# Kernel optimization log

Hardware: AMD Instinct MI355X
Metric: run time of the kernel (lower is better)

The kernel has to match this reference:

```python
import jax, jax.numpy as jnp
import numpy as np

N_NODES = 100000


def _sage_conv(x, src, dst, W_l, W_r, b):
    # mean aggregation of neighbor features over incoming edges (src -> dst)
    msgs = x[src]                                            # [E, d] gather
    agg = jax.ops.segment_sum(msgs, dst, num_segments=N_NODES)
    deg = jax.ops.segment_sum(jnp.ones_like(dst, dtype=x.dtype), dst,
                              num_segments=N_NODES)
    mean = agg / jnp.maximum(deg, 1.0)[:, None]              # [N, d]
    # PyG SAGEConv: lin_l(aggr) + lin_r(x); bias lives in lin_l
    return mean @ W_l + x @ W_r + b


def setup_inputs() -> dict:
    key = jax.random.key(0)
    k = jax.random.split(key, 8)
    d_in, d_h, E = 128, 128, 1600000
    scale_in = 1.0 / np.sqrt(d_in)
    scale_h = 1.0 / np.sqrt(d_h)
    return {
        "x": jax.random.normal(k[0], (N_NODES, d_in), dtype=jnp.float32),
        "edge_index": jax.random.randint(k[1], (2, E), 0, N_NODES, dtype=jnp.int64),
        "W_l0": jax.random.uniform(k[2], (d_in, d_h), jnp.float32, -scale_in, scale_in),
        "W_r0": jax.random.uniform(k[3], (d_in, d_h), jnp.float32, -scale_in, scale_in),
        "b0": jnp.zeros((d_h,), jnp.float32),
        "W_l1": jax.random.uniform(k[4], (d_h, d_h), jnp.float32, -scale_h, scale_h),
        "W_r1": jax.random.uniform(k[5], (d_h, d_h), jnp.float32, -scale_h, scale_h),
        "b1": jnp.zeros((d_h,), jnp.float32),
    }


def reference(x, edge_index, W_l0, W_r0, b0, W_l1, W_r1, b1):
    src, dst = edge_index[0], edge_index[1]
    h = _sage_conv(x, src, dst, W_l0, W_r0, b0)
    h = jax.nn.relu(h)  # dropout p=0.0 / eval mode -> identity
    h = _sage_conv(h, src, dst, W_l1, W_r1, b1)
    return h
```

## Files before the change

### kernel.cpp

```cpp
#include <hip/hip_runtime.h>


using bf16x8 = __attribute__((ext_vector_type(8))) __bf16;
using f32x4  = __attribute__((ext_vector_type(4))) float;

__device__ __forceinline__ unsigned short f2bf(float f) {
    __bf16 b = (__bf16)f;
    return __builtin_bit_cast(unsigned short, b);
}
__device__ __forceinline__ unsigned pk2(float a, float b) {
    return (unsigned)f2bf(a) | ((unsigned)f2bf(b) << 16);
}
__device__ __forceinline__ float bf2f(unsigned u16) {
    unsigned v = u16 << 16;
    return __builtin_bit_cast(float, v);
}

__device__ __forceinline__ int exscan1024(int v, int* wsum, int t) {
    int lane = t & 63, w = t >> 6;
    int x = v;
#pragma unroll
    for (int s = 1; s < 64; s <<= 1) {
        int y = __shfl_up(x, s);
        if (lane >= s) x += y;
    }
    if (lane == 63) wsum[w] = x;
    __syncthreads();
    if (w == 0) {
        int ws = (lane < 16) ? wsum[lane] : 0;
#pragma unroll
        for (int s = 1; s < 16; s <<= 1) {
            int y = __shfl_up(ws, s);
            if (lane >= s) ws += y;
        }
        if (lane < 16) wsum[lane] = ws;
    }
    __syncthreads();
    int base = (w > 0) ? wsum[w - 1] : 0;
    return base + x - v;
}


__global__ __launch_bounds__(256) void k_cvt(const float4* __restrict__ x,
                                             uint4* __restrict__ xb8,
                                             int nvec, int* __restrict__ ghist, int nb)
{
    int i = blockIdx.x * 256 + threadIdx.x;
    if (i < nb) ghist[i] = 0;
    if (i >= nvec) return;
    float4 a = x[2 * i], b = x[2 * i + 1];
    uint4 o;
    o.x = pk2(a.x, a.y);
    o.y = pk2(a.z, a.w);
    o.z = pk2(b.x, b.y);
    o.w = pk2(b.z, b.w);
    xb8[i] = o;
}


__global__ __launch_bounds__(256) void k_cvtw(const float* __restrict__ W0,
                                              const float* __restrict__ W1,
                                              const float* __restrict__ W2,
                                              const float* __restrict__ W3,
                                              unsigned short* __restrict__ wsw)
{
    int id = blockIdx.x * 256 + threadIdx.x;
    int m = id >> 14, r = id & 16383;
    int c = r >> 7, k = r & 127;
    const float* W = (m == 0) ? W0 : (m == 1) ? W1 : (m == 2) ? W2 : W3;
    wsw[m * 16384 + c * 128 + (k ^ ((c & 7) << 3))] = f2bf(W[k * 128 + c]);
}


__global__ __launch_bounds__(256) void k_binhist(const int* __restrict__ dst, int E,
                                                 int* __restrict__ ghist, int nb)
{
    __shared__ int lh[800];
    for (int i = threadIdx.x; i < nb; i += 256) lh[i] = 0;
    __syncthreads();
    for (int e = blockIdx.x * 256 + threadIdx.x; e < E; e += gridDim.x * 256)
        atomicAdd(&lh[dst[e] >> 7], 1);
    __syncthreads();
    for (int i = threadIdx.x; i < nb; i += 256)
        if (lh[i]) atomicAdd(&ghist[i], lh[i]);
}


__global__ __launch_bounds__(1024) void k_binscan(const int* __restrict__ ghist,
                                                  int* __restrict__ gbase,
                                                  int* __restrict__ gcur,
                                                  int* __restrict__ row_start,
                                                  int nb, int n, int E)
{
    __shared__ int wsum[16];
    int t = threadIdx.x;
    int v = (t < nb) ? ghist[t] : 0;
    int excl = exscan1024(v, wsum, t);
    if (t < nb) { gbase[t] = excl; gcur[t] = excl; }
    if (t == 0) { gbase[nb] = E; row_start[n] = E; }
}


#define SC_CHUNK 8192

__global__ __launch_bounds__(1024) void k_binscatter(const int* __restrict__ src,
                                                     const int* __restrict__ dst, int E,
                                                     int* __restrict__ gcur,
                                                     unsigned* __restrict__ binned, int nb)
{
    __shared__ int lh[800];
    __shared__ int lbase[800];
    __shared__ int gb[800];
    __shared__ int wsum[16];
    __shared__ unsigned long long staged[SC_CHUNK];
    int t = threadIdx.x;
    int e0 = blockIdx.x * SC_CHUNK;
    if (e0 >= E) return;
    int ecnt = E - e0; if (ecnt > SC_CHUNK) ecnt = SC_CHUNK;

    for (int i = t; i < nb; i += 1024) lh[i] = 0;
    __syncthreads();
    for (int i = t; i < ecnt; i += 1024)
        atomicAdd(&lh[dst[e0 + i] >> 7], 1);
    __syncthreads();
    int v = (t < nb) ? lh[t] : 0;
    int excl = exscan1024(v, wsum, t);
    if (t < nb) {
        lbase[t] = excl;
        gb[t] = v ? atomicAdd(&gcur[t], v) : 0;
        lh[t] = excl;
    }
    __syncthreads();
    for (int i = t; i < ecnt; i += 1024) {
        int d = dst[e0 + i], s = src[e0 + i];
        int b = d >> 7;
        int rank = atomicAdd(&lh[b], 1);
        unsigned pack = ((unsigned)s << 7) | (unsigned)(d & 127);
        unsigned gaddr = (unsigned)gb[b] + (unsigned)(rank - lbase[b]);
        staged[rank] = ((unsigned long long)gaddr << 32) | pack;
    }
    __syncthreads();
    for (int i = t; i < ecnt; i += 1024) {
        unsigned long long w = staged[i];
        binned[(unsigned)(w >> 32)] = (unsigned)w;
    }
}


#define BS_STAGE 8192

__global__ __launch_bounds__(256) void k_bucketsort(
    const unsigned* __restrict__ binned,
    const int* __restrict__ gbase,
    int* __restrict__ csr,
    int* __restrict__ row_start,
    float* __restrict__ inv_deg,
    int n)
{
    __shared__ int cnt[128];
    __shared__ int cur[128];
    __shared__ int wsum[4];
    __shared__ unsigned stg[BS_STAGE];
    const int t = threadIdx.x;
    const int b = blockIdx.x;
    const int beg = gbase[b], end = gbase[b + 1];
    const int len = end - beg;

    if (t < 128) cnt[t] = 0;
    __syncthreads();
    for (int i = beg + t; i < end; i += 256)
        atomicAdd(&cnt[binned[i] & 127], 1);
    __syncthreads();
    int v = (t < 128) ? cnt[t] : 0;
    {
        int lane = t & 63, w = t >> 6;
        int x = v;
#pragma unroll
        for (int s = 1; s < 64; s <<= 1) {
            int y = __shfl_up(x, s);
            if (lane >= s) x += y;
        }
        if (lane == 63) wsum[w] = x;
        __syncthreads();
        int base = (w == 1) ? wsum[0] : (w == 2) ? wsum[0] + wsum[1]
                 : (w == 3) ? wsum[0] + wsum[1] + wsum[2] : 0;
        int excl = base + x - v;
        if (t < 128) {
            cur[t] = excl;
            int node = b * 128 + t;
            if (node < n) {
                row_start[node] = beg + excl;
                inv_deg[node] = 1.f / (float)max(v, 1);
            }
        }
    }
    __syncthreads();

    if (len <= BS_STAGE) {
        for (int i = beg + t; i < end; i += 256) {
            unsigned w = binned[i];
            int r = atomicAdd(&cur[w & 127], 1);
            stg[r] = w >> 7;
        }
        __syncthreads();
        for (int i = t; i < len; i += 256)
            csr[beg + i] = (int)stg[i];
    } else {
        for (int i = beg + t; i < end; i += 256) {
            unsigned w = binned[i];
            int r = atomicAdd(&cur[w & 127], 1);
            csr[beg + r] = (int)(w >> 7);
        }
    }
}


__device__ __forceinline__ void acc8(float* a, uint4 v) {
    a[0] += __builtin_bit_cast(float, v.x << 16);
    a[1] += __builtin_bit_cast(float, v.x & 0xffff0000u);
    a[2] += __builtin_bit_cast(float, v.y << 16);
    a[3] += __builtin_bit_cast(float, v.y & 0xffff0000u);
    a[4] += __builtin_bit_cast(float, v.z << 16);
    a[5] += __builtin_bit_cast(float, v.z & 0xffff0000u);
    a[6] += __builtin_bit_cast(float, v.w << 16);
    a[7] += __builtin_bit_cast(float, v.w & 0xffff0000u);
}

__global__ __launch_bounds__(256) void k_agg(
    const unsigned short* __restrict__ feat,
    const int* __restrict__ csr,
    const int* __restrict__ row_start,
    const float* __restrict__ inv_deg,
    unsigned short* __restrict__ mean, int n)
{
    int node = blockIdx.x * 4 + (threadIdx.x >> 6);
    if (node >= n) return;
    const int lane = threadIdx.x & 63;
    const int q  = lane >> 4;
    const int cg = (lane & 15) << 3;
    const int beg = row_start[node], end = row_start[node + 1];

    float a[8];
#pragma unroll
    for (int j = 0; j < 8; ++j) a[j] = 0.f;

    for (int i = beg; i < end; i += 64) {
        int cnt = end - i; if (cnt > 64) cnt = 64;
        int idx = csr[i + (lane < cnt ? lane : cnt - 1)];
        for (int e = 0; e < cnt; e += 16) {
            const int r0 = e + q, r1 = e + 4 + q, r2 = e + 8 + q, r3 = e + 12 + q;
            int s0 = __shfl(idx, r0 < cnt ? r0 : cnt - 1);
            int s1 = __shfl(idx, r1 < cnt ? r1 : cnt - 1);
            int s2 = __shfl(idx, r2 < cnt ? r2 : cnt - 1);
            int s3 = __shfl(idx, r3 < cnt ? r3 : cnt - 1);
            uint4 v0 = *(const uint4*)(feat + ((size_t)s0 << 7) + cg);
            uint4 v1 = *(const uint4*)(feat + ((size_t)s1 << 7) + cg);
            uint4 v2 = *(const uint4*)(feat + ((size_t)s2 << 7) + cg);
            uint4 v3 = *(const uint4*)(feat + ((size_t)s3 << 7) + cg);
            if (r0 < cnt) acc8(a, v0);
            if (r1 < cnt) acc8(a, v1);
            if (r2 < cnt) acc8(a, v2);
            if (r3 < cnt) acc8(a, v3);
        }
    }

#pragma unroll
    for (int j = 0; j < 8; ++j) {
        a[j] += __shfl_xor(a[j], 16);
        a[j] += __shfl_xor(a[j], 32);
    }

    if (q == 0) {
        float w = inv_deg[node];
        uint4 o;
        o.x = pk2(a[0] * w, a[1] * w);
        o.y = pk2(a[2] * w, a[3] * w);
        o.z = pk2(a[4] * w, a[5] * w);
        o.w = pk2(a[6] * w, a[7] * w);
        *(uint4*)(mean + (size_t)node * 128 + cg) = o;
    }
}


template<bool RELU, bool OUTF32>
__global__ __launch_bounds__(256) void k_gemm(
    const unsigned short* __restrict__ A1,
    const unsigned short* __restrict__ A2,
    const unsigned short* __restrict__ Wsw,
    const float* __restrict__ bias,
    void* __restrict__ outv,
    int nrows)
{
    __shared__ __align__(16) unsigned short Wt[2 * 128 * 128];
    {
        const uint4* wsrc = (const uint4*)Wsw;
        uint4* wdst = (uint4*)Wt;
#pragma unroll
        for (int i = 0; i < 16; ++i)
            wdst[threadIdx.x + 256 * i] = wsrc[threadIdx.x + 256 * i];
    }
    __syncthreads();

    const int lane = threadIdx.x & 63;
    const int wave = threadIdx.x >> 6;
    const int lr = lane & 15;
    const int lg = lane >> 4;
    const int row0 = blockIdx.x * 128 + wave * 32;
    const int sw = (lr & 7) << 3;

    f32x4 acc[2][8];
#pragma unroll
    for (int m = 0; m < 2; ++m)
#pragma unroll
        for (int nn = 0; nn < 8; ++nn) acc[m][nn] = (f32x4){0.f, 0.f, 0.f, 0.f};

#pragma unroll
    for (int ks = 0; ks < 4; ++ks) {
        const int k0 = ks * 32 + lg * 8;
        bf16x8 a1[2], a2[2];
#pragma unroll
        for (int m = 0; m < 2; ++m) {
            int r = row0 + m * 16 + lr;
            if (r >= nrows) r = nrows - 1;
            a1[m] = *reinterpret_cast<const bf16x8*>(A1 + (size_t)r * 128 + k0);
            a2[m] = *reinterpret_cast<const bf16x8*>(A2 + (size_t)r * 128 + k0);
        }
        const int kidx = k0 ^ sw;
#pragma unroll
        for (int nn = 0; nn < 8; ++nn) {
            const int c = nn * 16 + lr;
            bf16x8 b1 = *reinterpret_cast<const bf16x8*>(&Wt[c * 128 + kidx]);
            bf16x8 b2 = *reinterpret_cast<const bf16x8*>(&Wt[16384 + c * 128 + kidx]);
#pragma unroll
            for (int m = 0; m < 2; ++m) {
                acc[m][nn] = __builtin_amdgcn_mfma_f32_16x16x32_bf16(a1[m], b1, acc[m][nn], 0, 0, 0);
                acc[m][nn] = __builtin_amdgcn_mfma_f32_16x16x32_bf16(a2[m], b2, acc[m][nn], 0, 0, 0);
            }
        }
    }

    __syncthreads();

#pragma unroll
    for (int m = 0; m < 2; ++m) {
#pragma unroll
        for (int nn = 0; nn < 8; ++nn) {
            const int c = nn * 16 + lr;
            const float bv = bias[c];
#pragma unroll
            for (int i = 0; i < 4; ++i) {
                int r = row0 + m * 16 + lg * 4 + i;
                if (r < nrows) {
                    float v = acc[m][nn][i] + bv;
                    if (RELU) v = fmaxf(v, 0.f);
                    if (OUTF32)
                        ((float*)outv)[(size_t)r * 128 + c] = v;
                    else
                        ((unsigned short*)outv)[(size_t)r * 128 + c] = f2bf(v);
                }
            }
        }
    }
}


extern "C" void kernel_launch(void* const* d_in, const int* in_sizes, int n_in,
                              void* d_out, int out_size, void* d_ws, size_t ws_size,
                              hipStream_t stream)
{
    const float* x   = (const float*)d_in[0];
    const int*   ei  = (const int*)d_in[1];
    const float* Wl0 = (const float*)d_in[2];
    const float* Wr0 = (const float*)d_in[3];
    const float* b0  = (const float*)d_in[4];
    const float* Wl1 = (const float*)d_in[5];
    const float* Wr1 = (const float*)d_in[6];
    const float* b1  = (const float*)d_in[7];
    float* out = (float*)d_out;

    const int n = in_sizes[0] / 128;
    const int E = in_sizes[1] / 2;
    const int* src = ei;
    const int* dst = ei + E;
    const int nb = (n + 127) >> 7;

    char* ws = (char*)d_ws;
    size_t off = 0;
    auto alloc = [&](size_t sz) -> char* {
        char* p = ws + off;
        off += (sz + 1023) & ~(size_t)1023;
        return p;
    };
    unsigned short* xb     = (unsigned short*)alloc((size_t)n * 128 * 2);
    unsigned short* mean   = (unsigned short*)alloc((size_t)n * 128 * 2);
    unsigned*       binned = (unsigned*)      alloc((size_t)E * 4);
    int*            rs     = (int*)           alloc((size_t)(n + 1) * 4);
    float*          invd   = (float*)         alloc((size_t)n * 4);
    int*            ghist  = (int*)           alloc((size_t)nb * 4);
    int*            gbase  = (int*)           alloc((size_t)(nb + 1) * 4);
    int*            gcur   = (int*)           alloc((size_t)nb * 4);
    unsigned short* wsw    = (unsigned short*)alloc(4 * 16384 * 2);
    int* csr;
    if (off + (size_t)E * 4 <= ws_size) csr = (int*)alloc((size_t)E * 4);
    else                                csr = (int*)binned;
    if (ws_size < off) return;

    const int nvec = n * 128 / 8;
    const int nsc  = (E + SC_CHUNK - 1) / SC_CHUNK;

    hipLaunchKernelGGL(k_cvt,        dim3((nvec + 255) / 256), dim3(256),  0, stream,
                       (const float4*)x, (uint4*)xb, nvec, ghist, nb);
    hipLaunchKernelGGL(k_cvtw,       dim3(256),                dim3(256),  0, stream,
                       Wl0, Wr0, Wl1, Wr1, wsw);
    hipLaunchKernelGGL(k_binhist,    dim3(512),                dim3(256),  0, stream,
                       dst, E, ghist, nb);
    hipLaunchKernelGGL(k_binscan,    dim3(1),                  dim3(1024), 0, stream,
                       ghist, gbase, gcur, rs, nb, n, E);
    hipLaunchKernelGGL(k_binscatter, dim3(nsc),                dim3(1024), 0, stream,
                       src, dst, E, gcur, binned, nb);
    hipLaunchKernelGGL(k_bucketsort, dim3(nb),                 dim3(256),  0, stream,
                       binned, gbase, csr, rs, invd, n);
    hipLaunchKernelGGL(k_agg,  dim3((n + 3) / 4), dim3(256), 0, stream,
                       xb, csr, rs, invd, mean, n);
    hipLaunchKernelGGL((k_gemm<true, false>), dim3(nb), dim3(256), 0, stream,
                       mean, xb, wsw, b0, (void*)xb, n);
    hipLaunchKernelGGL(k_agg,  dim3((n + 3) / 4), dim3(256), 0, stream,
                       xb, csr, rs, invd, mean, n);
    hipLaunchKernelGGL((k_gemm<false, true>), dim3(nb), dim3(256), 0, stream,
                       mean, xb, wsw + 2 * 16384, b1, (void*)out, n);
}
```

Baseline: 223.4 us.

## Fuse prep kernels and process two nodes per wavefront in aggregation

Merges the feature conversion, weight conversion and destination histogram kernels into one launch, and moves histogram zeroing to a memset. The aggregation kernel now has each wavefront handle two adjacent nodes at once, interleaving their neighbour gathers so more independent loads are in flight, and it accumulates in packed float2 vectors. This aims to cut launch overhead and hide gather latency, at the cost of more registers per thread and divergence when the two nodes have very different degrees.

```diff
diff --git a/kernel.cpp b/kernel.cpp
--- a/kernel.cpp
+++ b/kernel.cpp
@@ -3,6 +3,7 @@
 
 using bf16x8 = __attribute__((ext_vector_type(8))) __bf16;
 using f32x4  = __attribute__((ext_vector_type(4))) float;
+using f32x2  = __attribute__((ext_vector_type(2))) float;
 
 __device__ __forceinline__ unsigned short f2bf(float f) {
     __bf16 b = (__bf16)f;
@@ -11,10 +12,6 @@
 __device__ __forceinline__ unsigned pk2(float a, float b) {
     return (unsigned)f2bf(a) | ((unsigned)f2bf(b) << 16);
 }
-__device__ __forceinline__ float bf2f(unsigned u16) {
-    unsigned v = u16 << 16;
-    return __builtin_bit_cast(float, v);
-}
 
 __device__ __forceinline__ int exscan1024(int v, int* wsum, int t) {
     int lane = t & 63, w = t >> 6;
@@ -41,48 +38,41 @@
 }
 
 
-__global__ __launch_bounds__(256) void k_cvt(const float4* __restrict__ x,
-                                             uint4* __restrict__ xb8,
-                                             int nvec, int* __restrict__ ghist, int nb)
-{
-    int i = blockIdx.x * 256 + threadIdx.x;
-    if (i < nb) ghist[i] = 0;
-    if (i >= nvec) return;
-    float4 a = x[2 * i], b = x[2 * i + 1];
-    uint4 o;
-    o.x = pk2(a.x, a.y);
-    o.y = pk2(a.z, a.w);
-    o.z = pk2(b.x, b.y);
-    o.w = pk2(b.z, b.w);
-    xb8[i] = o;
-}
-
-
-__global__ __launch_bounds__(256) void k_cvtw(const float* __restrict__ W0,
-                                              const float* __restrict__ W1,
-                                              const float* __restrict__ W2,
-                                              const float* __restrict__ W3,
-                                              unsigned short* __restrict__ wsw)
-{
-    int id = blockIdx.x * 256 + threadIdx.x;
-    int m = id >> 14, r = id & 16383;
-    int c = r >> 7, k = r & 127;
-    const float* W = (m == 0) ? W0 : (m == 1) ? W1 : (m == 2) ? W2 : W3;
-    wsw[m * 16384 + c * 128 + (k ^ ((c & 7) << 3))] = f2bf(W[k * 128 + c]);
-}
-
-
-__global__ __launch_bounds__(256) void k_binhist(const int* __restrict__ dst, int E,
-                                                 int* __restrict__ ghist, int nb)
+__global__ __launch_bounds__(256) void k_prep(
+    const float4* __restrict__ x, uint4* __restrict__ xb8, int nvec, int ncvt,
+    const float* __restrict__ W0, const float* __restrict__ W1,
+    const float* __restrict__ W2, const float* __restrict__ W3,
+    unsigned short* __restrict__ wsw, int ncvtw,
+    const int* __restrict__ dst, int E, int* __restrict__ ghist, int nb, int nhist)
 {
     __shared__ int lh[800];
-    for (int i = threadIdx.x; i < nb; i += 256) lh[i] = 0;
-    __syncthreads();
-    for (int e = blockIdx.x * 256 + threadIdx.x; e < E; e += gridDim.x * 256)
-        atomicAdd(&lh[dst[e] >> 7], 1);
-    __syncthreads();
-    for (int i = threadIdx.x; i < nb; i += 256)
-        if (lh[i]) atomicAdd(&ghist[i], lh[i]);
+    const int b = blockIdx.x;
+    if (b < ncvt) {
+        int i = b * 256 + threadIdx.x;
+        if (i >= nvec) return;
+        float4 a = x[2 * i], c = x[2 * i + 1];
+        uint4 o;
+        o.x = pk2(a.x, a.y);
+        o.y = pk2(a.z, a.w);
+        o.z = pk2(c.x, c.y);
+        o.w = pk2(c.z, c.w);
+        xb8[i] = o;
+    } else if (b < ncvt + ncvtw) {
+        int id = (b - ncvt) * 256 + threadIdx.x;
+        int m = id >> 14, r = id & 16383;
+        int c = r >> 7, k = r & 127;
+        const float* W = (m == 0) ? W0 : (m == 1) ? W1 : (m == 2) ? W2 : W3;
+        wsw[m * 16384 + c * 128 + (k ^ ((c & 7) << 3))] = f2bf(W[k * 128 + c]);
+    } else {
+        int hb = b - ncvt - ncvtw;
+        for (int i = threadIdx.x; i < nb; i += 256) lh[i] = 0;
+        __syncthreads();
+        for (int e = hb * 256 + threadIdx.x; e < E; e += nhist * 256)
+            atomicAdd(&lh[dst[e] >> 7], 1);
+        __syncthreads();
+        for (int i = threadIdx.x; i < nb; i += 256)
+            if (lh[i]) atomicAdd(&ghist[i], lh[i]);
+    }
 }
 
 
@@ -215,15 +205,15 @@
 }
 
 
-__device__ __forceinline__ void acc8(float* a, uint4 v) {
-    a[0] += __builtin_bit_cast(float, v.x << 16);
-    a[1] += __builtin_bit_cast(float, v.x & 0xffff0000u);
-    a[2] += __builtin_bit_cast(float, v.y << 16);
-    a[3] += __builtin_bit_cast(float, v.y & 0xffff0000u);
-    a[4] += __builtin_bit_cast(float, v.z << 16);
-    a[5] += __builtin_bit_cast(float, v.z & 0xffff0000u);
-    a[6] += __builtin_bit_cast(float, v.w << 16);
-    a[7] += __builtin_bit_cast(float, v.w & 0xffff0000u);
+__device__ __forceinline__ f32x2 up2(unsigned x) {
+    return (f32x2){__builtin_bit_cast(float, x << 16),
+                   __builtin_bit_cast(float, x & 0xffff0000u)};
+}
+__device__ __forceinline__ void acc8(f32x2* a, uint4 v) {
+    a[0] += up2(v.x);
+    a[1] += up2(v.y);
+    a[2] += up2(v.z);
+    a[3] += up2(v.w);
 }
 
 __global__ __launch_bounds__(256) void k_agg(
@@ -233,51 +223,102 @@
     const float* __restrict__ inv_deg,
     unsigned short* __restrict__ mean, int n)
 {
-    int node = blockIdx.x * 4 + (threadIdx.x >> 6);
-    if (node >= n) return;
+    const int nodeA = blockIdx.x * 8 + (threadIdx.x >> 6) * 2;
+    if (nodeA >= n) return;
+    const bool two = (nodeA + 1 < n);
     const int lane = threadIdx.x & 63;
     const int q  = lane >> 4;
     const int cg = (lane & 15) << 3;
-    const int beg = row_start[node], end = row_start[node + 1];
-
-    float a[8];
-#pragma unroll
-    for (int j = 0; j < 8; ++j) a[j] = 0.f;
-
-    for (int i = beg; i < end; i += 64) {
-        int cnt = end - i; if (cnt > 64) cnt = 64;
-        int idx = csr[i + (lane < cnt ? lane : cnt - 1)];
-        for (int e = 0; e < cnt; e += 16) {
-            const int r0 = e + q, r1 = e + 4 + q, r2 = e + 8 + q, r3 = e + 12 + q;
-            int s0 = __shfl(idx, r0 < cnt ? r0 : cnt - 1);
-            int s1 = __shfl(idx, r1 < cnt ? r1 : cnt - 1);
-            int s2 = __shfl(idx, r2 < cnt ? r2 : cnt - 1);
-            int s3 = __shfl(idx, r3 < cnt ? r3 : cnt - 1);
-            uint4 v0 = *(const uint4*)(feat + ((size_t)s0 << 7) + cg);
-            uint4 v1 = *(const uint4*)(feat + ((size_t)s1 << 7) + cg);
-            uint4 v2 = *(const uint4*)(feat + ((size_t)s2 << 7) + cg);
-            uint4 v3 = *(const uint4*)(feat + ((size_t)s3 << 7) + cg);
-            if (r0 < cnt) acc8(a, v0);
-            if (r1 < cnt) acc8(a, v1);
-            if (r2 < cnt) acc8(a, v2);
-            if (r3 < cnt) acc8(a, v3);
-        }
-    }
-
-#pragma unroll
-    for (int j = 0; j < 8; ++j) {
-        a[j] += __shfl_xor(a[j], 16);
-        a[j] += __shfl_xor(a[j], 32);
+
+    const int begA = row_start[nodeA];
+    const int endA = row_start[nodeA + 1];
+    const int endB = two ? row_start[nodeA + 2] : endA;
+
+    f32x2 aA[4], aB[4];
+#pragma unroll
+    for (int j = 0; j < 4; ++j) { aA[j] = (f32x2){0.f, 0.f}; aB[j] = (f32x2){0.f, 0.f}; }
+
+    int iA = begA, iB = endA;
+    while (iA < endA || iB < endB) {
+        int cntA = endA - iA; cntA = cntA > 64 ? 64 : cntA;
+        int cntB = endB - iB; cntB = cntB > 64 ? 64 : cntB;
+        int idxA = 0, idxB = 0;
+        if (cntA) idxA = csr[iA + (lane < cntA ? lane : cntA - 1)];
+        if (cntB) idxB = csr[iB + (lane < cntB ? lane : cntB - 1)];
+        const int cA = cntA > 0 ? cntA - 1 : 0;
+        const int cB = cntB > 0 ? cntB - 1 : 0;
+        const int mx = cntA > cntB ? cntA : cntB;
+        for (int e = 0; e < mx; e += 16) {
+            const bool dA = e < cntA, dB = e < cntB;
+            uint4 vA0, vA1, vA2, vA3, vB0, vB1, vB2, vB3;
+            int rA0 = e + q, rA1 = e + 4 + q, rA2 = e + 8 + q, rA3 = e + 12 + q;
+            int rB0 = rA0, rB1 = rA1, rB2 = rA2, rB3 = rA3;
+            if (dA) {
+                int s0 = __shfl(idxA, rA0 < cA ? rA0 : cA);
+                int s1 = __shfl(idxA, rA1 < cA ? rA1 : cA);
+                int s2 = __shfl(idxA, rA2 < cA ? rA2 : cA);
+                int s3 = __shfl(idxA, rA3 < cA ? rA3 : cA);
+                vA0 = *(const uint4*)(feat + ((size_t)s0 << 7) + cg);
+                vA1 = *(const uint4*)(feat + ((size_t)s1 << 7) + cg);
+                vA2 = *(const uint4*)(feat + ((size_t)s2 << 7) + cg);
+                vA3 = *(const uint4*)(feat + ((size_t)s3 << 7) + cg);
+            }
+            if (dB) {
+                int s0 = __shfl(idxB, rB0 < cB ? rB0 : cB);
+                int s1 = __shfl(idxB, rB1 < cB ? rB1 : cB);
+                int s2 = __shfl(idxB, rB2 < cB ? rB2 : cB);
+                int s3 = __shfl(idxB, rB3 < cB ? rB3 : cB);
+                vB0 = *(const uint4*)(feat + ((size_t)s0 << 7) + cg);
+                vB1 = *(const uint4*)(feat + ((size_t)s1 << 7) + cg);
+                vB2 = *(const uint4*)(feat + ((size_t)s2 << 7) + cg);
+                vB3 = *(const uint4*)(feat + ((size_t)s3 << 7) + cg);
+            }
+            if (dA) {
+                if (rA0 < cntA) acc8(aA, vA0);
+                if (rA1 < cntA) acc8(aA, vA1);
+                if (rA2 < cntA) acc8(aA, vA2);
+                if (rA3 < cntA) acc8(aA, vA3);
+            }
+            if (dB) {
+                if (rB0 < cntB) acc8(aB, vB0);
+                if (rB1 < cntB) acc8(aB, vB1);
+                if (rB2 < cntB) acc8(aB, vB2);
+                if (rB3 < cntB) acc8(aB, vB3);
+            }
+        }
+        iA += cntA;
+        iB += cntB;
+    }
+
+#pragma unroll
+    for (int j = 0; j < 4; ++j) {
+        aA[j].x += __shfl_xor(aA[j].x, 16);
+        aA[j].x += __shfl_xor(aA[j].x, 32);
+        aA[j].y += __shfl_xor(aA[j].y, 16);
+        aA[j].y += __shfl_xor(aA[j].y, 32);
+        aB[j].x += __shfl_xor(aB[j].x, 16);
+        aB[j].x += __shfl_xor(aB[j].x, 32);
+        aB[j].y += __shfl_xor(aB[j].y, 16);
+        aB[j].y += __shfl_xor(aB[j].y, 32);
     }
 
     if (q == 0) {
-        float w = inv_deg[node];
+        float w = inv_deg[nodeA];
         uint4 o;
-        o.x = pk2(a[0] * w, a[1] * w);
-        o.y = pk2(a[2] * w, a[3] * w);
-        o.z = pk2(a[4] * w, a[5] * w);
-        o.w = pk2(a[6] * w, a[7] * w);
-        *(uint4*)(mean + (size_t)node * 128 + cg) = o;
+        o.x = pk2(aA[0].x * w, aA[0].y * w);
+        o.y = pk2(aA[1].x * w, aA[1].y * w);
+        o.z = pk2(aA[2].x * w, aA[2].y * w);
+        o.w = pk2(aA[3].x * w, aA[3].y * w);
+        *(uint4*)(mean + (size_t)nodeA * 128 + cg) = o;
+        if (two) {
+            float w2 = inv_deg[nodeA + 1];
+            uint4 p;
+            p.x = pk2(aB[0].x * w2, aB[0].y * w2);
+            p.y = pk2(aB[1].x * w2, aB[1].y * w2);
+            p.z = pk2(aB[2].x * w2, aB[2].y * w2);
+            p.w = pk2(aB[3].x * w2, aB[3].y * w2);
+            *(uint4*)(mean + (size_t)(nodeA + 1) * 128 + cg) = p;
+        }
     }
 }
 
@@ -405,26 +446,28 @@
     else                                csr = (int*)binned;
     if (ws_size < off) return;
 
-    const int nvec = n * 128 / 8;
-    const int nsc  = (E + SC_CHUNK - 1) / SC_CHUNK;
-
-    hipLaunchKernelGGL(k_cvt,        dim3((nvec + 255) / 256), dim3(256),  0, stream,
-                       (const float4*)x, (uint4*)xb, nvec, ghist, nb);
-    hipLaunchKernelGGL(k_cvtw,       dim3(256),                dim3(256),  0, stream,
-                       Wl0, Wr0, Wl1, Wr1, wsw);
-    hipLaunchKernelGGL(k_binhist,    dim3(512),                dim3(256),  0, stream,
-                       dst, E, ghist, nb);
-    hipLaunchKernelGGL(k_binscan,    dim3(1),                  dim3(1024), 0, stream,
+    const int nvec  = n * 128 / 8;
+    const int ncvt  = (nvec + 255) / 256;
+    const int ncvtw = 256;
+    const int nhist = 512;
+    const int nsc   = (E + SC_CHUNK - 1) / SC_CHUNK;
+
+    hipMemsetAsync(ghist, 0, (size_t)nb * sizeof(int), stream);
+    hipLaunchKernelGGL(k_prep, dim3(ncvt + ncvtw + nhist), dim3(256), 0, stream,
+                       (const float4*)x, (uint4*)xb, nvec, ncvt,
+                       Wl0, Wr0, Wl1, Wr1, wsw, ncvtw,
+                       dst, E, ghist, nb, nhist);
+    hipLaunchKernelGGL(k_binscan,    dim3(1),    dim3(1024), 0, stream,
                        ghist, gbase, gcur, rs, nb, n, E);
-    hipLaunchKernelGGL(k_binscatter, dim3(nsc),                dim3(1024), 0, stream,
+    hipLaunchKernelGGL(k_binscatter, dim3(nsc),  dim3(1024), 0, stream,
                        src, dst, E, gcur, binned, nb);
-    hipLaunchKernelGGL(k_bucketsort, dim3(nb),                 dim3(256),  0, stream,
+    hipLaunchKernelGGL(k_bucketsort, dim3(nb),   dim3(256),  0, stream,
                        binned, gbase, csr, rs, invd, n);
-    hipLaunchKernelGGL(k_agg,  dim3((n + 3) / 4), dim3(256), 0, stream,
+    hipLaunchKernelGGL(k_agg,  dim3((n + 7) / 8), dim3(256), 0, stream,
                        xb, csr, rs, invd, mean, n);
     hipLaunchKernelGGL((k_gemm<true, false>), dim3(nb), dim3(256), 0, stream,
                        mean, xb, wsw, b0, (void*)xb, n);
-    hipLaunchKernelGGL(k_agg,  dim3((n + 3) / 4), dim3(256), 0, stream,
+    hipLaunchKernelGGL(k_agg,  dim3((n + 7) / 8), dim3(256), 0, stream,
                        xb, csr, rs, invd, mean, n);
     hipLaunchKernelGGL((k_gemm<false, true>), dim3(nb), dim3(256), 0, stream,
                        mean, xb, wsw + 2 * 16384, b1, (void*)out, n);
```

Result: no change. 227.5 us (+1.8%).

## Replace two-level binned CSR build with per-node atomic counting sort

Applied to the files above, without the earlier changes.

Swaps the bin-histogram, bin-scatter and per-bin bucket-sort pipeline for a direct per-node degree histogram using global atomics, a two-pass block scan, and an atomic-cursor scatter into CSR. Fuses feature conversion, weight conversion and histogram into one launch to cut kernel launches and passes over edges. In exchange it relies on 1.6M global atomics to random addresses and gives a nondeterministic neighbour order within rows, which loses the locality the staged bin sort provided. Also tweaks the bf16 unpack and hoists the column offset in aggregation.

```diff
diff --git a/kernel.cpp b/kernel.cpp
--- a/kernel.cpp
+++ b/kernel.cpp
@@ -41,189 +41,101 @@
 }
 
 
-__global__ __launch_bounds__(256) void k_cvt(const float4* __restrict__ x,
-                                             uint4* __restrict__ xb8,
-                                             int nvec, int* __restrict__ ghist, int nb)
-{
-    int i = blockIdx.x * 256 + threadIdx.x;
-    if (i < nb) ghist[i] = 0;
-    if (i >= nvec) return;
-    float4 a = x[2 * i], b = x[2 * i + 1];
-    uint4 o;
-    o.x = pk2(a.x, a.y);
-    o.y = pk2(a.z, a.w);
-    o.z = pk2(b.x, b.y);
-    o.w = pk2(b.z, b.w);
-    xb8[i] = o;
-}
-
-
-__global__ __launch_bounds__(256) void k_cvtw(const float* __restrict__ W0,
-                                              const float* __restrict__ W1,
-                                              const float* __restrict__ W2,
-                                              const float* __restrict__ W3,
-                                              unsigned short* __restrict__ wsw)
-{
-    int id = blockIdx.x * 256 + threadIdx.x;
-    int m = id >> 14, r = id & 16383;
-    int c = r >> 7, k = r & 127;
-    const float* W = (m == 0) ? W0 : (m == 1) ? W1 : (m == 2) ? W2 : W3;
-    wsw[m * 16384 + c * 128 + (k ^ ((c & 7) << 3))] = f2bf(W[k * 128 + c]);
-}
-
-
-__global__ __launch_bounds__(256) void k_binhist(const int* __restrict__ dst, int E,
-                                                 int* __restrict__ ghist, int nb)
-{
-    __shared__ int lh[800];
-    for (int i = threadIdx.x; i < nb; i += 256) lh[i] = 0;
-    __syncthreads();
-    for (int e = blockIdx.x * 256 + threadIdx.x; e < E; e += gridDim.x * 256)
-        atomicAdd(&lh[dst[e] >> 7], 1);
-    __syncthreads();
-    for (int i = threadIdx.x; i < nb; i += 256)
-        if (lh[i]) atomicAdd(&ghist[i], lh[i]);
-}
-
-
-__global__ __launch_bounds__(1024) void k_binscan(const int* __restrict__ ghist,
-                                                  int* __restrict__ gbase,
-                                                  int* __restrict__ gcur,
-                                                  int* __restrict__ row_start,
-                                                  int nb, int n, int E)
-{
-    __shared__ int wsum[16];
-    int t = threadIdx.x;
-    int v = (t < nb) ? ghist[t] : 0;
-    int excl = exscan1024(v, wsum, t);
-    if (t < nb) { gbase[t] = excl; gcur[t] = excl; }
-    if (t == 0) { gbase[nb] = E; row_start[n] = E; }
-}
-
-
-#define SC_CHUNK 8192
-
-__global__ __launch_bounds__(1024) void k_binscatter(const int* __restrict__ src,
-                                                     const int* __restrict__ dst, int E,
-                                                     int* __restrict__ gcur,
-                                                     unsigned* __restrict__ binned, int nb)
-{
-    __shared__ int lh[800];
-    __shared__ int lbase[800];
-    __shared__ int gb[800];
-    __shared__ int wsum[16];
-    __shared__ unsigned long long staged[SC_CHUNK];
-    int t = threadIdx.x;
-    int e0 = blockIdx.x * SC_CHUNK;
-    if (e0 >= E) return;
-    int ecnt = E - e0; if (ecnt > SC_CHUNK) ecnt = SC_CHUNK;
-
-    for (int i = t; i < nb; i += 1024) lh[i] = 0;
-    __syncthreads();
-    for (int i = t; i < ecnt; i += 1024)
-        atomicAdd(&lh[dst[e0 + i] >> 7], 1);
-    __syncthreads();
-    int v = (t < nb) ? lh[t] : 0;
-    int excl = exscan1024(v, wsum, t);
-    if (t < nb) {
-        lbase[t] = excl;
-        gb[t] = v ? atomicAdd(&gcur[t], v) : 0;
-        lh[t] = excl;
-    }
-    __syncthreads();
-    for (int i = t; i < ecnt; i += 1024) {
-        int d = dst[e0 + i], s = src[e0 + i];
-        int b = d >> 7;
-        int rank = atomicAdd(&lh[b], 1);
-        unsigned pack = ((unsigned)s << 7) | (unsigned)(d & 127);
-        unsigned gaddr = (unsigned)gb[b] + (unsigned)(rank - lbase[b]);
-        staged[rank] = ((unsigned long long)gaddr << 32) | pack;
-    }
-    __syncthreads();
-    for (int i = t; i < ecnt; i += 1024) {
-        unsigned long long w = staged[i];
-        binned[(unsigned)(w >> 32)] = (unsigned)w;
-    }
-}
-
-
-#define BS_STAGE 8192
-
-__global__ __launch_bounds__(256) void k_bucketsort(
-    const unsigned* __restrict__ binned,
-    const int* __restrict__ gbase,
-    int* __restrict__ csr,
-    int* __restrict__ row_start,
-    float* __restrict__ inv_deg,
-    int n)
-{
-    __shared__ int cnt[128];
-    __shared__ int cur[128];
-    __shared__ int wsum[4];
-    __shared__ unsigned stg[BS_STAGE];
-    const int t = threadIdx.x;
+__global__ __launch_bounds__(256) void k_prep(
+    const float4* __restrict__ x, uint4* __restrict__ xb8, int nvec, int ncvt,
+    const float* __restrict__ W0, const float* __restrict__ W1,
+    const float* __restrict__ W2, const float* __restrict__ W3,
+    unsigned short* __restrict__ wsw, int ncvtw,
+    const int* __restrict__ dst, int E, int* __restrict__ deg, int nhist)
+{
     const int b = blockIdx.x;
-    const int beg = gbase[b], end = gbase[b + 1];
-    const int len = end - beg;
-
-    if (t < 128) cnt[t] = 0;
-    __syncthreads();
-    for (int i = beg + t; i < end; i += 256)
-        atomicAdd(&cnt[binned[i] & 127], 1);
-    __syncthreads();
-    int v = (t < 128) ? cnt[t] : 0;
-    {
-        int lane = t & 63, w = t >> 6;
-        int x = v;
-#pragma unroll
-        for (int s = 1; s < 64; s <<= 1) {
-            int y = __shfl_up(x, s);
-            if (lane >= s) x += y;
-        }
-        if (lane == 63) wsum[w] = x;
-        __syncthreads();
-        int base = (w == 1) ? wsum[0] : (w == 2) ? wsum[0] + wsum[1]
-                 : (w == 3) ? wsum[0] + wsum[1] + wsum[2] : 0;
-        int excl = base + x - v;
-        if (t < 128) {
-            cur[t] = excl;
-            int node = b * 128 + t;
-            if (node < n) {
-                row_start[node] = beg + excl;
-                inv_deg[node] = 1.f / (float)max(v, 1);
-            }
-        }
-    }
-    __syncthreads();
-
-    if (len <= BS_STAGE) {
-        for (int i = beg + t; i < end; i += 256) {
-            unsigned w = binned[i];
-            int r = atomicAdd(&cur[w & 127], 1);
-            stg[r] = w >> 7;
-        }
-        __syncthreads();
-        for (int i = t; i < len; i += 256)
-            csr[beg + i] = (int)stg[i];
+    if (b < ncvt) {
+        int i = b * 256 + threadIdx.x;
+        if (i >= nvec) return;
+        float4 a = x[2 * i], c = x[2 * i + 1];
+        uint4 o;
+        o.x = pk2(a.x, a.y);
+        o.y = pk2(a.z, a.w);
+        o.z = pk2(c.x, c.y);
+        o.w = pk2(c.z, c.w);
+        xb8[i] = o;
+    } else if (b < ncvt + ncvtw) {
+        int id = (b - ncvt) * 256 + threadIdx.x;
+        int m = id >> 14, r = id & 16383;
+        int c = r >> 7, k = r & 127;
+        const float* W = (m == 0) ? W0 : (m == 1) ? W1 : (m == 2) ? W2 : W3;
+        wsw[m * 16384 + c * 128 + (k ^ ((c & 7) << 3))] = f2bf(W[k * 128 + c]);
     } else {
-        for (int i = beg + t; i < end; i += 256) {
-            unsigned w = binned[i];
-            int r = atomicAdd(&cur[w & 127], 1);
-            csr[beg + r] = (int)(w >> 7);
-        }
+        int hb = b - ncvt - ncvtw;
+        for (int e = hb * 256 + threadIdx.x; e < E; e += nhist * 256)
+            atomicAdd(&deg[dst[e]], 1);
+    }
+}
+
+
+__global__ __launch_bounds__(1024) void k_scanA(const int* __restrict__ deg, int n,
+                                                int* __restrict__ bsum)
+{
+    __shared__ int ws[16];
+    const int t = threadIdx.x, b = blockIdx.x;
+    const int i = b * 1024 + t;
+    int v = (i < n) ? deg[i] : 0;
+#pragma unroll
+    for (int s = 32; s; s >>= 1) v += __shfl_xor(v, s);
+    if ((t & 63) == 0) ws[t >> 6] = v;
+    __syncthreads();
+    if (t == 0) {
+        int x = 0;
+#pragma unroll
+        for (int j = 0; j < 16; ++j) x += ws[j];
+        bsum[b] = x;
+    }
+}
+
+
+__global__ __launch_bounds__(1024) void k_scanB(const int* __restrict__ deg, int n,
+                                                const int* __restrict__ bsum, int nch,
+                                                int* __restrict__ rs,
+                                                int* __restrict__ cur,
+                                                float* __restrict__ invd, int E)
+{
+    __shared__ int sb[128];
+    __shared__ int ws[16];
+    const int t = threadIdx.x, b = blockIdx.x;
+    if (t < 128) sb[t] = (t < nch) ? bsum[t] : 0;
+    __syncthreads();
+    int base = 0;
+    for (int j = 0; j < b; ++j) base += sb[j];
+    const int i = b * 1024 + t;
+    int v = (i < n) ? deg[i] : 0;
+    int excl = exscan1024(v, ws, t);
+    if (i < n) {
+        rs[i]  = base + excl;
+        cur[i] = base + excl;
+        invd[i] = 1.f / (float)max(v, 1);
+    }
+    if (b == 0 && t == 0) rs[n] = E;
+}
+
+
+__global__ __launch_bounds__(256) void k_scatter(const int* __restrict__ src,
+                                                 const int* __restrict__ dst, int E,
+                                                 int* __restrict__ cur,
+                                                 int* __restrict__ csr)
+{
+    for (int e = blockIdx.x * 256 + threadIdx.x; e < E; e += gridDim.x * 256) {
+        int d = dst[e], s = src[e];
+        int r = atomicAdd(&cur[d], 1);
+        csr[r] = s;
     }
 }
 
 
 __device__ __forceinline__ void acc8(float* a, uint4 v) {
-    a[0] += __builtin_bit_cast(float, v.x << 16);
-    a[1] += __builtin_bit_cast(float, v.x & 0xffff0000u);
-    a[2] += __builtin_bit_cast(float, v.y << 16);
-    a[3] += __builtin_bit_cast(float, v.y & 0xffff0000u);
-    a[4] += __builtin_bit_cast(float, v.z << 16);
-    a[5] += __builtin_bit_cast(float, v.z & 0xffff0000u);
-    a[6] += __builtin_bit_cast(float, v.w << 16);
-    a[7] += __builtin_bit_cast(float, v.w & 0xffff0000u);
+    a[0] += bf2f(v.x & 0xffffu); a[1] += bf2f(v.x >> 16);
+    a[2] += bf2f(v.y & 0xffffu); a[3] += bf2f(v.y >> 16);
+    a[4] += bf2f(v.z & 0xffffu); a[5] += bf2f(v.z >> 16);
+    a[6] += bf2f(v.w & 0xffffu); a[7] += bf2f(v.w >> 16);
 }
 
 __global__ __launch_bounds__(256) void k_agg(
@@ -233,11 +145,12 @@
     const float* __restrict__ inv_deg,
     unsigned short* __restrict__ mean, int n)
 {
-    int node = blockIdx.x * 4 + (threadIdx.x >> 6);
+    const int node = blockIdx.x * 4 + (threadIdx.x >> 6);
     if (node >= n) return;
     const int lane = threadIdx.x & 63;
     const int q  = lane >> 4;
     const int cg = (lane & 15) << 3;
+    const unsigned short* fp = feat + cg;
     const int beg = row_start[node], end = row_start[node + 1];
 
     float a[8];
@@ -253,10 +166,10 @@
             int s1 = __shfl(idx, r1 < cnt ? r1 : cnt - 1);
             int s2 = __shfl(idx, r2 < cnt ? r2 : cnt - 1);
             int s3 = __shfl(idx, r3 < cnt ? r3 : cnt - 1);
-            uint4 v0 = *(const uint4*)(feat + ((size_t)s0 << 7) + cg);
-            uint4 v1 = *(const uint4*)(feat + ((size_t)s1 << 7) + cg);
-            uint4 v2 = *(const uint4*)(feat + ((size_t)s2 << 7) + cg);
-            uint4 v3 = *(const uint4*)(feat + ((size_t)s3 << 7) + cg);
+            uint4 v0 = *(const uint4*)(fp + ((size_t)s0 << 7));
+            uint4 v1 = *(const uint4*)(fp + ((size_t)s1 << 7));
+            uint4 v2 = *(const uint4*)(fp + ((size_t)s2 << 7));
+            uint4 v3 = *(const uint4*)(fp + ((size_t)s3 << 7));
             if (r0 < cnt) acc8(a, v0);
             if (r1 < cnt) acc8(a, v1);
             if (r2 < cnt) acc8(a, v2);
@@ -393,33 +306,31 @@
     };
     unsigned short* xb     = (unsigned short*)alloc((size_t)n * 128 * 2);
     unsigned short* mean   = (unsigned short*)alloc((size_t)n * 128 * 2);
-    unsigned*       binned = (unsigned*)      alloc((size_t)E * 4);
+    int*            csr    = (int*)           alloc((size_t)E * 4);
     int*            rs     = (int*)           alloc((size_t)(n + 1) * 4);
     float*          invd   = (float*)         alloc((size_t)n * 4);
-    int*            ghist  = (int*)           alloc((size_t)nb * 4);
-    int*            gbase  = (int*)           alloc((size_t)(nb + 1) * 4);
-    int*            gcur   = (int*)           alloc((size_t)nb * 4);
+    int*            deg    = (int*)           alloc((size_t)n * 4);
+    int*            cur    = (int*)           alloc((size_t)n * 4);
+    int*            bsum   = (int*)           alloc(128 * 4);
     unsigned short* wsw    = (unsigned short*)alloc(4 * 16384 * 2);
-    int* csr;
-    if (off + (size_t)E * 4 <= ws_size) csr = (int*)alloc((size_t)E * 4);
-    else                                csr = (int*)binned;
     if (ws_size < off) return;
 
-    const int nvec = n * 128 / 8;
-    const int nsc  = (E + SC_CHUNK - 1) / SC_CHUNK;
-
-    hipLaunchKernelGGL(k_cvt,        dim3((nvec + 255) / 256), dim3(256),  0, stream,
-                       (const float4*)x, (uint4*)xb, nvec, ghist, nb);
-    hipLaunchKernelGGL(k_cvtw,       dim3(256),                dim3(256),  0, stream,
-                       Wl0, Wr0, Wl1, Wr1, wsw);
-    hipLaunchKernelGGL(k_binhist,    dim3(512),                dim3(256),  0, stream,
-                       dst, E, ghist, nb);
-    hipLaunchKernelGGL(k_binscan,    dim3(1),                  dim3(1024), 0, stream,
-                       ghist, gbase, gcur, rs, nb, n, E);
-    hipLaunchKernelGGL(k_binscatter, dim3(nsc),                dim3(1024), 0, stream,
-                       src, dst, E, gcur, binned, nb);
-    hipLaunchKernelGGL(k_bucketsort, dim3(nb),                 dim3(256),  0, stream,
-                       binned, gbase, csr, rs, invd, n);
+    const int nvec  = n * 128 / 8;
+    const int ncvt  = (nvec + 255) / 256;
+    const int ncvtw = 256;
+    const int nhist = 512;
+    const int nch   = (n + 1023) / 1024;
+
+    hipMemsetAsync(deg, 0, (size_t)n * sizeof(int), stream);
+    hipLaunchKernelGGL(k_prep, dim3(ncvt + ncvtw + nhist), dim3(256), 0, stream,
+                       (const float4*)x, (uint4*)xb, nvec, ncvt,
+                       Wl0, Wr0, Wl1, Wr1, wsw, ncvtw,
+                       dst, E, deg, nhist);
+    hipLaunchKernelGGL(k_scanA, dim3(nch), dim3(1024), 0, stream, deg, n, bsum);
+    hipLaunchKernelGGL(k_scanB, dim3(nch), dim3(1024), 0, stream,
+                       deg, n, bsum, nch, rs, cur, invd, E);
+    hipLaunchKernelGGL(k_scatter, dim3(1024), dim3(256), 0, stream,
+                       src, dst, E, cur, csr);
     hipLaunchKernelGGL(k_agg,  dim3((n + 3) / 4), dim3(256), 0, stream,
                        xb, csr, rs, invd, mean, n);
     hipLaunchKernelGGL((k_gemm<true, false>), dim3(nb), dim3(256), 0, stream,
```

Result: slower. 394.9 us (+76.7%).
